# Optimization experiments

Hardware: AMD Instinct MI355X
Metric: run time of the kernel (lower is better)

The kernel has to match this reference:

```python
import jax, jax.numpy as jnp
import numpy as np


def setup_inputs() -> dict:
    key = jax.random.key(0)
    k1, k2, k3 = jax.random.split(key, 3)
    x = jax.random.normal(k1, (32, 256, 56, 56), dtype=jnp.float32)
    att_w = jax.random.normal(k2, (4, 256), dtype=jnp.float32) * 0.05  # 1x1 attention conv weight (K, Cin)
    weight = jax.random.normal(k3, (4, 256, 256, 3, 3), dtype=jnp.float32) * 0.05  # (K, Cout, Cin, kh, kw)
    return {"x": x, "att_w": att_w, "weight": weight}


def reference(x, att_w, weight):
    # x: (B, Cin, H, W); att_w: (K, Cin); weight: (K, Cout, Cin, kh, kw)
    # Attention: global avg pool -> 1x1 conv (Cin->K) -> sigmoid  (named softmax_att but is sigmoid)
    pooled = jnp.mean(x, axis=(2, 3))                 # (B, Cin)
    att = jax.nn.sigmoid(pooled @ att_w.T)            # (B, K)
    # Per-sample expert-mixed conv kernels
    agg_w = jnp.einsum('bk,koihw->boihw', att, weight)  # (B, Cout, Cin, kh, kw)

    def conv_one(xi, wi):
        # xi: (Cin, H, W), wi: (Cout, Cin, kh, kw)
        return jax.lax.conv_general_dilated(
            xi[None], wi,
            window_strides=(1, 1),
            padding=[(1, 1), (1, 1)],
            rhs_dilation=(1, 1),
            dimension_numbers=('NCHW', 'OIHW', 'NCHW'),
        )[0]

    out = jax.vmap(conv_one)(x, agg_w)                # (B, Cout, H, W)
    return out
```

## Files before the change

kernel.cpp:

```cpp
#include <hip/hip_runtime.h>

typedef __attribute__((ext_vector_type(8))) short short8;
typedef __attribute__((ext_vector_type(4))) float floatx4;

__device__ __forceinline__ unsigned short bf16_rne(float f) {
  unsigned int u = __builtin_bit_cast(unsigned int, f);
  u += 0x7fffu + ((u >> 16) & 1u);
  return (unsigned short)(u >> 16);
}

__device__ __forceinline__ void glds16(const void* g, void* l) {
  __builtin_amdgcn_global_load_lds((const __attribute__((address_space(1))) void*)g,
                                   (__attribute__((address_space(3))) void*)l, 16, 0, 0);
}


__global__ void zero_pk_kernel(float* __restrict__ pk) {
  pk[threadIdx.x] = 0.f;
}

__global__ __launch_bounds__(256) void prep_kernel(const float* __restrict__ x,
                                                   const float* __restrict__ att_w,
                                                   unsigned short* __restrict__ xpad,
                                                   float* __restrict__ pooledk) {
  const int bid = blockIdx.x;
  const int b   = bid / 196;
  const int rem = bid - b * 196;
  const int cig = rem / 49;
  const int spc = rem - cig * 49;
  const int t  = threadIdx.x;
  const int cs = t >> 6, sl = t & 63;
  const int sp0 = spc * 64;

  __shared__ unsigned short T2[64 * 72];
  __shared__ float red[4][4];

  const float* xrow = x + (size_t)(b * 256 + cig * 64 + cs * 16) * 3136 + sp0 + sl;
  float v[16];
  #pragma unroll
  for (int i = 0; i < 16; ++i) v[i] = xrow[(size_t)i * 3136];

  float acc0 = 0.f, acc1 = 0.f, acc2 = 0.f, acc3 = 0.f;
  #pragma unroll
  for (int i = 0; i < 16; ++i) {
    const int ci = cig * 64 + cs * 16 + i;
    acc0 += v[i] * att_w[0 * 256 + ci];
    acc1 += v[i] * att_w[1 * 256 + ci];
    acc2 += v[i] * att_w[2 * 256 + ci];
    acc3 += v[i] * att_w[3 * 256 + ci];
  }
  #pragma unroll
  for (int o = 32; o > 0; o >>= 1) {
    acc0 += __shfl_xor(acc0, o, 64);
    acc1 += __shfl_xor(acc1, o, 64);
    acc2 += __shfl_xor(acc2, o, 64);
    acc3 += __shfl_xor(acc3, o, 64);
  }
  if (sl == 0) { red[cs][0] = acc0; red[cs][1] = acc1; red[cs][2] = acc2; red[cs][3] = acc3; }

  short8 w0, w1;
  #pragma unroll
  for (int i = 0; i < 8; ++i) w0[i] = (short)bf16_rne(v[i]);
  #pragma unroll
  for (int i = 0; i < 8; ++i) w1[i] = (short)bf16_rne(v[8 + i]);
  *(short8*)(T2 + sl * 72 + cs * 16) = w0;
  *(short8*)(T2 + sl * 72 + cs * 16 + 8) = w1;
  __syncthreads();

  if (t < 4) {
    float s = red[0][t] + red[1][t] + red[2][t] + red[3][t];
    atomicAdd(&pooledk[b * 4 + t], s);
  }

  unsigned short* xb = xpad + (size_t)b * (8 * 3364 * 32);
  #pragma unroll
  for (int it = 0; it < 2; ++it) {
    const int c9 = it * 256 + t;
    const int o2 = c9 & 3, spl = (c9 >> 2) & 63, kcsel = c9 >> 8;
    const int kc = cig * 2 + kcsel;
    const int spg = sp0 + spl;
    const int h = spg / 56, wc = spg - h * 56;
    const int pos = (h + 1) * 58 + (wc + 1);
    const short8 vv = *(const short8*)(T2 + spl * 72 + (kcsel * 4 + o2) * 8);
    *(short8*)(xb + (size_t)kc * (3364 * 32) + pos * 32 + o2 * 8) = vv;
  }

  if (cig == 0 && spc < 4) {
    const short8 z = {0, 0, 0, 0, 0, 0, 0, 0};
    #pragma unroll
    for (int it = 0; it < 8; ++it) {
      const int idx = it * 256 + t;
      if (idx >= 1824) break;
      const int s8 = idx & 3, kc = (idx >> 2) & 7, j = idx >> 5;
      const int pi = spc * 57 + j;
      int h2, w2;
      if (pi < 58)       { h2 = 0;  w2 = pi; }
      else if (pi < 116) { h2 = 57; w2 = pi - 58; }
      else { const int k = pi - 116; h2 = 1 + (k >> 1); w2 = (k & 1) * 57; }
      *(short8*)(xb + (size_t)kc * (3364 * 32) + (h2 * 58 + w2) * 32 + s8 * 8) = z;
    }
  }
}

__global__ __launch_bounds__(256) void agg_kernel(const float* __restrict__ w,
                                                  const float* __restrict__ pooledk,
                                                  unsigned short* __restrict__ agg) {
  const int co = blockIdx.x;
  const int bq = blockIdx.y;
  const int t = threadIdx.x;
  __shared__ float W[4][2304];
  __shared__ float attl[16];
  if (t < 16) {
    const float z = pooledk[bq * 16 + t] * (1.f / 3136.f);
    attl[t] = 1.f / (1.f + expf(-z));
  }
  #pragma unroll
  for (int e = 0; e < 4; ++e) {
    const float* src = w + (size_t)(e * 256 + co) * 2304;
    #pragma unroll
    for (int j = 0; j < 9; ++j) W[e][j * 256 + t] = src[j * 256 + t];
  }
  __syncthreads();

  #pragma unroll
  for (int rep = 0; rep < 2; ++rep) {
    const int id = rep * 256 + t;
    if (id < 288) {
      const int kc  = id / 36;
      const int rm  = id - kc * 36;
      const int rs  = rm >> 2;
      const int oct = rm & 3;
      const int wib = (kc * 32 + oct * 8) * 9 + rs;
      const int off = (kc * 9 + rs) * 8192 + co * 32 + oct * 8;
      float w0[8], w1[8], w2[8], w3[8];
      #pragma unroll
      for (int u = 0; u < 8; ++u) {
        w0[u] = W[0][wib + u * 9];
        w1[u] = W[1][wib + u * 9];
        w2[u] = W[2][wib + u * 9];
        w3[u] = W[3][wib + u * 9];
      }
      #pragma unroll
      for (int bl = 0; bl < 4; ++bl) {
        const int b = bq * 4 + bl;
        const float a0 = attl[bl * 4 + 0], a1 = attl[bl * 4 + 1];
        const float a2 = attl[bl * 4 + 2], a3 = attl[bl * 4 + 3];
        short8 vv;
        #pragma unroll
        for (int u = 0; u < 8; ++u)
          vv[u] = (short)bf16_rne(a0 * w0[u] + a1 * w1[u] + a2 * w2[u] + a3 * w3[u]);
        *(short8*)(agg + (size_t)b * 589824 + off) = vv;
      }
    }
  }
}

__global__ __launch_bounds__(256, 3) void conv_kernel(const unsigned short* __restrict__ xpad,
                                                      const unsigned short* __restrict__ aggw,
                                                      float* __restrict__ out) {
  __shared__ alignas(16) unsigned short Bsm[2][348 * 32];

  const int t  = threadIdx.x;
  const int bx0 = blockIdx.x;
  const int bx  = (bx0 & 7) * 200 + (bx0 >> 3);
  const int p_t  = bx % 25;
  const int co_t = (bx / 25) & 1;
  const int b    = bx / 50;
  const int p0   = p_t * 128;
  const int oh_min = p0 / 56;

  const unsigned short* xb  = xpad + (size_t)b * (8 * 3364 * 32);
  const unsigned short* awb = aggw + (size_t)b * 589824 + co_t * 4096;

  const int lane = t & 63;
  const int wv = t >> 6;
  const int wm = wv >> 1;
  const int wn = wv & 1;
  const int m16 = lane & 15;
  const int q = lane >> 4;

  int aoff[4], brow[4];
  #pragma unroll
  for (int i = 0; i < 4; ++i)
    aoff[i] = (wm * 64 + i * 16 + m16) * 32 + q * 8;
  #pragma unroll
  for (int j = 0; j < 4; ++j) {
    const int pf = p0 + wn * 64 + j * 16 + m16;
    const int oh = pf / 56;
    const int ow = pf - oh * 56;
    brow[j] = ((oh - oh_min) * 58 + ow) * 32 + q * 8;
  }

  int bofO[6];
  #pragma unroll
  for (int i = 0; i < 6; ++i) {
    const int c = i * 256 + t;
    if (c < 1392) {
      const int pos = c >> 2, sub = c & 3;
      const int prow = pos / 58, pcol = pos - prow * 58;
      int ih2 = oh_min + prow; if (ih2 > 57) ih2 = 57;
      bofO[i] = (ih2 * 58 + pcol) * 32 + sub * 8;
    } else bofO[i] = -1;
  }

  floatx4 acc[4][4];
  #pragma unroll
  for (int i = 0; i < 4; ++i)
    #pragma unroll
    for (int j = 0; j < 4; ++j)
      acc[i][j] = (floatx4){0.f, 0.f, 0.f, 0.f};

  #pragma unroll
  for (int i = 0; i < 6; ++i)
    if (bofO[i] >= 0) glds16(xb + bofO[i], (void*)(Bsm[0] + (i * 256 + t) * 8));
  __syncthreads();

  for (int kc = 0; kc < 8; ++kc) {
    const unsigned short* Bcur = Bsm[kc & 1];
    unsigned short* Bnxt = Bsm[(kc + 1) & 1];
    const unsigned short* xnxt = xb + (size_t)(kc + 1) * (3364 * 32);
    const unsigned short* aslab = awb + (size_t)kc * 73728;
    const bool doB = (kc < 7);

    short8 afc[4], afn[4];
    #pragma unroll
    for (int i = 0; i < 4; ++i)
      afc[i] = *(const short8*)(aslab + aoff[i]);

    #pragma unroll
    for (int rs = 0; rs < 9; ++rs) {
      if (rs < 8) {
        #pragma unroll
        for (int i = 0; i < 4; ++i)
          afn[i] = *(const short8*)(aslab + (size_t)(rs + 1) * 8192 + aoff[i]);
      }
      __builtin_amdgcn_sched_barrier(0);
      if (rs < 6 && doB && bofO[rs] >= 0)
        glds16(xnxt + bofO[rs], (void*)(Bnxt + (rs * 256 + t) * 8));
      __builtin_amdgcn_sched_barrier(0);

      const int r = rs / 3, s = rs - r * 3;
      const int d = (r * 58 + s) * 32;
      short8 bfr[4];
      #pragma unroll
      for (int j = 0; j < 4; ++j)
        bfr[j] = *(const short8*)(Bcur + brow[j] + d);
      __builtin_amdgcn_s_setprio(1);
      #pragma unroll
      for (int i = 0; i < 4; ++i)
        #pragma unroll
        for (int j = 0; j < 4; ++j)
          acc[i][j] = __builtin_amdgcn_mfma_f32_16x16x32_bf16(afc[i], bfr[j], acc[i][j], 0, 0, 0);
      __builtin_amdgcn_s_setprio(0);

      if (rs < 8) {
        #pragma unroll
        for (int i = 0; i < 4; ++i) afc[i] = afn[i];
      }
    }
    __syncthreads();
  }

  #pragma unroll
  for (int i = 0; i < 4; ++i) {
    const int co = co_t * 128 + wm * 64 + i * 16 + q * 4;
    float* orow = out + (size_t)(b * 256 + co) * 3136;
    #pragma unroll
    for (int j = 0; j < 4; ++j) {
      const int pp = p0 + wn * 64 + j * 16 + m16;
      if (pp < 3136) {
        #pragma unroll
        for (int rg = 0; rg < 4; ++rg)
          orow[(size_t)rg * 3136 + pp] = acc[i][j][rg];
      }
    }
  }
}

extern "C" void kernel_launch(void* const* d_in, const int* in_sizes, int n_in,
                              void* d_out, int out_size, void* d_ws, size_t ws_size,
                              hipStream_t stream) {
  const float* x      = (const float*)d_in[0];
  const float* att_w  = (const float*)d_in[1];
  const float* weight = (const float*)d_in[2];
  float* out = (float*)d_out;

  char* ws = (char*)d_ws;
  float* pooledk       = (float*)ws;
  unsigned short* agg  = (unsigned short*)(ws + 65536);
  unsigned short* xpad = (unsigned short*)(ws + 65536 + 37748736);

  zero_pk_kernel<<<1, 128, 0, stream>>>(pooledk);
  prep_kernel<<<6272, 256, 0, stream>>>(x, att_w, xpad, pooledk);
  agg_kernel<<<dim3(256, 8), 256, 0, stream>>>(weight, pooledk, agg);
  conv_kernel<<<1600, 256, 0, stream>>>(xpad, agg, out);
}
```

Measured before the change: 337.7 us.

## Deepen weight-fragment prefetch to three slabs with partial vmcnt waits

Weight fragments in the conv kernel are now prefetched three filter taps ahead through a rotating register queue, and the queue runs across channel-chunk boundaries instead of restarting each chunk. The full __syncthreads is replaced by an explicit s_waitcnt vmcnt(12) plus s_barrier, so the outstanding weight loads stay in flight while the LDS tile loads are waited on. The LDS tile is padded to 384 rows so the bounds guards on the global-to-LDS copies can go. The aim is to hide global weight-load latency and cut branch overhead, at the price of more VGPRs (possible occupancy loss at 3 waves) and some redundant loads past the last chunk.

```diff
diff --git a/kernel.cpp b/kernel.cpp
--- a/kernel.cpp
+++ b/kernel.cpp
@@ -158,7 +158,7 @@
 __global__ __launch_bounds__(256, 3) void conv_kernel(const unsigned short* __restrict__ xpad,
                                                       const unsigned short* __restrict__ aggw,
                                                       float* __restrict__ out) {
-  __shared__ alignas(16) unsigned short Bsm[2][348 * 32];
+  __shared__ alignas(16) unsigned short Bsm[2][384 * 32];
 
   const int t  = threadIdx.x;
   const int bx0 = blockIdx.x;
@@ -195,12 +195,10 @@
   #pragma unroll
   for (int i = 0; i < 6; ++i) {
     const int c = i * 256 + t;
-    if (c < 1392) {
-      const int pos = c >> 2, sub = c & 3;
-      const int prow = pos / 58, pcol = pos - prow * 58;
-      int ih2 = oh_min + prow; if (ih2 > 57) ih2 = 57;
-      bofO[i] = (ih2 * 58 + pcol) * 32 + sub * 8;
-    } else bofO[i] = -1;
+    const int pos = c >> 2, sub = c & 3;
+    const int prow = pos / 58, pcol = pos - prow * 58;
+    int ih2 = oh_min + prow; if (ih2 > 57) ih2 = 57;
+    bofO[i] = (ih2 * 58 + pcol) * 32 + sub * 8;
   }
 
   floatx4 acc[4][4];
@@ -212,30 +210,32 @@
 
   #pragma unroll
   for (int i = 0; i < 6; ++i)
-    if (bofO[i] >= 0) glds16(xb + bofO[i], (void*)(Bsm[0] + (i * 256 + t) * 8));
-  __syncthreads();
+    glds16(xb + bofO[i], (void*)(Bsm[0] + (i * 256 + t) * 8));
+  short8 af0[4], af1[4], af2[4];
+  #pragma unroll
+  for (int i = 0; i < 4; ++i) af0[i] = *(const short8*)(awb + (size_t)0 * 8192 + aoff[i]);
+  #pragma unroll
+  for (int i = 0; i < 4; ++i) af1[i] = *(const short8*)(awb + (size_t)1 * 8192 + aoff[i]);
+  #pragma unroll
+  for (int i = 0; i < 4; ++i) af2[i] = *(const short8*)(awb + (size_t)2 * 8192 + aoff[i]);
+  asm volatile("s_waitcnt vmcnt(12)" ::: "memory");
+  __builtin_amdgcn_s_barrier();
+  __builtin_amdgcn_sched_barrier(0);
 
   for (int kc = 0; kc < 8; ++kc) {
     const unsigned short* Bcur = Bsm[kc & 1];
     unsigned short* Bnxt = Bsm[(kc + 1) & 1];
-    const unsigned short* xnxt = xb + (size_t)(kc + 1) * (3364 * 32);
-    const unsigned short* aslab = awb + (size_t)kc * 73728;
-    const bool doB = (kc < 7);
-
-    short8 afc[4], afn[4];
-    #pragma unroll
-    for (int i = 0; i < 4; ++i)
-      afc[i] = *(const short8*)(aslab + aoff[i]);
+    const unsigned short* xnxt = xb + (size_t)((kc + 1) & 7) * (3364 * 32);
 
     #pragma unroll
     for (int rs = 0; rs < 9; ++rs) {
-      if (rs < 8) {
-        #pragma unroll
-        for (int i = 0; i < 4; ++i)
-          afn[i] = *(const short8*)(aslab + (size_t)(rs + 1) * 8192 + aoff[i]);
-      }
+      int pfs = kc * 9 + rs + 3; if (pfs > 71) pfs = 71;
+      short8 afN[4];
+      #pragma unroll
+      for (int i = 0; i < 4; ++i)
+        afN[i] = *(const short8*)(awb + (size_t)pfs * 8192 + aoff[i]);
       __builtin_amdgcn_sched_barrier(0);
-      if (rs < 6 && doB && bofO[rs] >= 0)
+      if (rs < 6)
         glds16(xnxt + bofO[rs], (void*)(Bnxt + (rs * 256 + t) * 8));
       __builtin_amdgcn_sched_barrier(0);
 
@@ -250,15 +250,15 @@
       for (int i = 0; i < 4; ++i)
         #pragma unroll
         for (int j = 0; j < 4; ++j)
-          acc[i][j] = __builtin_amdgcn_mfma_f32_16x16x32_bf16(afc[i], bfr[j], acc[i][j], 0, 0, 0);
+          acc[i][j] = __builtin_amdgcn_mfma_f32_16x16x32_bf16(af0[i], bfr[j], acc[i][j], 0, 0, 0);
       __builtin_amdgcn_s_setprio(0);
 
-      if (rs < 8) {
-        #pragma unroll
-        for (int i = 0; i < 4; ++i) afc[i] = afn[i];
-      }
-    }
-    __syncthreads();
+      #pragma unroll
+      for (int i = 0; i < 4; ++i) { af0[i] = af1[i]; af1[i] = af2[i]; af2[i] = afN[i]; }
+    }
+    asm volatile("s_waitcnt vmcnt(12)" ::: "memory");
+    __builtin_amdgcn_s_barrier();
+    __builtin_amdgcn_sched_barrier(0);
   }
 
   #pragma unroll
```

Result: slower. 385.1 us (+14.0%).
